# Kernel tuning notes

Hardware: AMD Instinct MI355X
Metric: run time of the kernel (lower is better)

Reference implementation:

```python
import jax, jax.numpy as jnp
import numpy as np
import math

B, N, D, H = 2, 2048, 512, 8
DH = D // H
HID = int(D * 16 / 3)  # 2730, SwiGLU hidden; chunks into 1365+1365
EPS = 1e-5


def _get_slopes(n):
    # n=8 is a power of two
    start = 2.0 ** (-2.0 ** (-(math.log2(n) - 3)))
    return np.array([start * (start ** i) for i in range(n)], dtype=np.float32)

_SLOPES = jnp.asarray(_get_slopes(H))  # [H]


def _ln(x, w, b):
    m = jnp.mean(x, axis=-1, keepdims=True)
    v = jnp.mean((x - m) ** 2, axis=-1, keepdims=True)
    return (x - m) * jax.lax.rsqrt(v + EPS) * w + b


def setup_inputs() -> dict:
    key = jax.random.key(0)
    ks = jax.random.split(key, 20)
    p = lambda k, s: jax.random.normal(k, s, jnp.float32) * 0.02
    return {
        "x": jax.random.normal(ks[0], (B, N, D), jnp.float32),
        "coords": jax.random.uniform(ks[1], (B, N, 2), jnp.float32) * 100.0,
        "q_w": p(ks[2], (D, D)), "q_b": jnp.zeros((D,), jnp.float32),
        "k_w": p(ks[3], (D, D)), "k_b": jnp.zeros((D,), jnp.float32),
        "v_w": p(ks[4], (D, D)), "v_b": jnp.zeros((D,), jnp.float32),
        "o_w": p(ks[5], (D, D)), "o_b": jnp.zeros((D,), jnp.float32),
        "gamma1": jnp.ones((D,), jnp.float32),
        "ln1_w": jnp.ones((D,), jnp.float32), "ln1_b": jnp.zeros((D,), jnp.float32),
        "fc1_w": p(ks[6], (HID, D)), "fc1_b": jnp.zeros((HID,), jnp.float32),
        "fc2_w": p(ks[7], (D, HID // 2)), "fc2_b": jnp.zeros((D,), jnp.float32),
        "gamma2": jnp.ones((D,), jnp.float32),
        "ln2_w": jnp.ones((D,), jnp.float32), "ln2_b": jnp.zeros((D,), jnp.float32),
    }


def reference(x, coords, q_w, q_b, k_w, k_b, v_w, v_b, o_w, o_b, gamma1,
              ln1_w, ln1_b, fc1_w, fc1_b, fc2_w, fc2_b, gamma2, ln2_w, ln2_b):
    # ---- residual1: distance-ALiBi attention (eval mode: x + gamma1*attn(norm(x)))
    xn = _ln(x, ln1_w, ln1_b)
    q = (xn @ q_w.T + q_b).reshape(B, N, H, DH).transpose(0, 2, 1, 3)  # [b,h,n,dh]
    k = (xn @ k_w.T + k_b).reshape(B, N, H, DH).transpose(0, 2, 1, 3)
    v = (xn @ v_w.T + v_b).reshape(B, N, H, DH).transpose(0, 2, 1, 3)
    # pairwise Euclidean distance of tile coords -> [b,n,n]
    diff = coords[:, :, None, :] - coords[:, None, :, :]
    dist = jnp.sqrt(jnp.sum(diff * diff, axis=-1))
    attn_bias = -_SLOPES[None, :, None, None] * dist[:, None, :, :]  # [b,h,n,n]
    scale = 1.0 / math.sqrt(DH)
    scores = jnp.einsum('bhqd,bhkd->bhqk', q, k) * scale + attn_bias
    attn = jax.nn.softmax(scores, axis=-1)
    ctx = jnp.einsum('bhqk,bhkd->bhqd', attn, v)
    ctx = ctx.transpose(0, 2, 1, 3).reshape(B, N, D)
    attn_out = ctx @ o_w.T + o_b
    x = x + gamma1 * attn_out
    # ---- residual2: SwiGLU-style MLP (eval mode: x + gamma2*mlp(norm(x)))
    xn2 = _ln(x, ln2_w, ln2_b)
    hpre = xn2 @ fc1_w.T + fc1_b  # [b,n,HID]
    h1, h2 = jnp.split(hpre, 2, axis=-1)
    mlp_out = (jax.nn.silu(h1) * h2) @ fc2_w.T + fc2_b
    return x + gamma2 * mlp_out
```

## Files before the change

### kernel.cpp

```cpp
#include <hip/hip_runtime.h>
#include <math.h>

#define Bdim  2
#define Nseq  2048
#define Dmod  512
#define Hn    8
#define DHd   64
#define HID   2730
#define HHALF 1365
#define HC    1408
#define NPACK 2816
#define ROWS  4096
#define NSPLIT 4
#define KT_PER (Nseq / 64 / NSPLIT)

typedef __bf16 bf16x8 __attribute__((ext_vector_type(8)));
typedef __bf16 bf16x4 __attribute__((ext_vector_type(4)));
typedef float  f32x4  __attribute__((ext_vector_type(4)));

__device__ __forceinline__ void glds16(const __bf16* g, __bf16* l) {
    __builtin_amdgcn_global_load_lds(
        (const __attribute__((address_space(1))) void*)g,
        (__attribute__((address_space(3))) void*)l, 16, 0, 0);
}

#define SEG0 (1536*512)
#define SEG1 (512*512)
#define SEG2 (NPACK*512)
#define SEG3 (512*HC)
__global__ __launch_bounds__(256) void convert_all(
    const float* __restrict__ q_w, const float* __restrict__ k_w,
    const float* __restrict__ v_w, const float* __restrict__ o_w,
    const float* __restrict__ fc1_w, const float* __restrict__ fc2_w,
    __bf16* __restrict__ wqkv, __bf16* __restrict__ wo,
    __bf16* __restrict__ wfc1p, __bf16* __restrict__ wfc2p)
{
    int idx = blockIdx.x * 256 + threadIdx.x;
    if (idx < SEG0) {
        int n = idx >> 9, k = idx & 511;
        float v = (n < 512) ? q_w[n * 512 + k]
                : (n < 1024) ? k_w[(n - 512) * 512 + k]
                : v_w[(n - 1024) * 512 + k];
        wqkv[idx] = (__bf16)v;
        return;
    }
    idx -= SEG0;
    if (idx < SEG1) { wo[idx] = (__bf16)o_w[idx]; return; }
    idx -= SEG1;
    if (idx < SEG2) {
        int n = idx >> 9, k = idx & 511;
        int j = n >> 5, u = n & 31;
        int base = j * 16 + (u & 15);
        float v = 0.0f;
        if (base < HHALF) {
            int hidx = base + ((u & 16) ? HHALF : 0);
            v = fc1_w[(size_t)hidx * 512 + k];
        }
        wfc1p[idx] = (__bf16)v;
        return;
    }
    idx -= SEG2;
    if (idx < SEG3) {
        int n = idx / HC, k = idx - n * HC;
        float v = (k < HHALF) ? fc2_w[(size_t)n * HHALF + k] : 0.0f;
        wfc2p[idx] = (__bf16)v;
    }
}

__global__ __launch_bounds__(256) void ln_kernel(
    const float* __restrict__ x, const float* __restrict__ w,
    const float* __restrict__ b, __bf16* __restrict__ out)
{
    const int row = blockIdx.x;
    const int tid = threadIdx.x;
    const float* xr = x + (size_t)row * Dmod;
    float2 v = *(const float2*)(xr + tid * 2);
    float s  = v.x + v.y;
    float sq = v.x * v.x + v.y * v.y;
#pragma unroll
    for (int m = 1; m < 64; m <<= 1) {
        s  += __shfl_xor(s, m, 64);
        sq += __shfl_xor(sq, m, 64);
    }
    __shared__ float ss[4], ssq[4];
    const int wv = tid >> 6;
    if ((tid & 63) == 0) { ss[wv] = s; ssq[wv] = sq; }
    __syncthreads();
    s  = ss[0] + ss[1] + ss[2] + ss[3];
    sq = ssq[0] + ssq[1] + ssq[2] + ssq[3];
    const float mean = s * (1.0f / Dmod);
    const float var  = sq * (1.0f / Dmod) - mean * mean;
    const float rstd = rsqrtf(var + 1e-5f);
    float2 wv2 = *(const float2*)(w + tid * 2);
    float2 bv2 = *(const float2*)(b + tid * 2);
    __bf16* orow = out + (size_t)row * Dmod + tid * 2;
    orow[0] = (__bf16)((v.x - mean) * rstd * wv2.x + bv2.x);
    orow[1] = (__bf16)((v.y - mean) * rstd * wv2.y + bv2.y);
}

__global__ __launch_bounds__(256) void gemm_res(
    const __bf16* __restrict__ A, int lda,
    const __bf16* __restrict__ Bw, int ldb,
    const float* __restrict__ bias, int K,
    float* __restrict__ out_f32, int ld_out,
    const float* __restrict__ res, const float* __restrict__ g)
{
    __shared__ __bf16 As[64 * 32];
    __shared__ __bf16 Bs[64 * 32];
    const int tid  = threadIdx.x;
    const int wave = tid >> 6, lane = tid & 63;
    const int t    = lane & 15, quad = lane >> 4;
    const int m0   = blockIdx.x * 64;
    const int n0   = blockIdx.y * 64;
    const int sr   = tid >> 2, sc = (tid & 3) * 8;

    f32x4 acc[4] = {};

    for (int k0 = 0; k0 < K; k0 += 32) {
        __syncthreads();
        glds16(A  + (size_t)(m0 + sr) * lda + k0 + sc, As + tid * 8);
        glds16(Bw + (size_t)(n0 + sr) * ldb + k0 + sc, Bs + tid * 8);
        __syncthreads();
        bf16x8 a = *(const bf16x8*)(As + (wave * 16 + t) * 32 + quad * 8);
#pragma unroll
        for (int ct = 0; ct < 4; ++ct) {
            bf16x8 b = *(const bf16x8*)(Bs + (ct * 16 + t) * 32 + quad * 8);
            acc[ct] = __builtin_amdgcn_mfma_f32_16x16x32_bf16(a, b, acc[ct], 0, 0, 0);
        }
    }

    const int row_base = m0 + wave * 16 + quad * 4;
#pragma unroll
    for (int ct = 0; ct < 4; ++ct) {
        const int col = n0 + ct * 16 + t;
        const float bb = bias[col];
#pragma unroll
        for (int r = 0; r < 4; ++r) {
            const int row = row_base + r;
            out_f32[(size_t)row * ld_out + col] =
                res[(size_t)row * ld_out + col] + g[col] * (acc[ct][r] + bb);
        }
    }
}

#define LDT 136
__global__ __launch_bounds__(256) void qkv_gemm128(
    const __bf16* __restrict__ A, const __bf16* __restrict__ W,
    const float* __restrict__ qb_, const float* __restrict__ kb_,
    const float* __restrict__ vb_,
    __bf16* __restrict__ qk, __bf16* __restrict__ vtg)
{
    __shared__ __bf16 smem[64 * LDT];
    __bf16* As = smem;
    __bf16* Bs = smem + 4096;
    const int tid  = threadIdx.x;
    const int wave = tid >> 6, lane = tid & 63;
    const int t    = lane & 15, quad = lane >> 4;
    const int m0   = blockIdx.x * 128, n0 = blockIdx.y * 128;
    const int mr   = (wave & 1) * 64,  nr = (wave >> 1) * 64;
    const int ra0 = tid >> 2,          ca0 = (tid & 3) * 8;
    const int ra1 = (tid + 256) >> 2,  ca1 = (tid & 3) * 8;

    f32x4 acc[4][4] = {};

    for (int k0 = 0; k0 < Dmod; k0 += 32) {
        __syncthreads();
        glds16(A + (size_t)(m0 + ra0) * Dmod + k0 + ca0, As + tid * 8);
        glds16(A + (size_t)(m0 + ra1) * Dmod + k0 + ca1, As + (tid + 256) * 8);
        glds16(W + (size_t)(n0 + ra0) * Dmod + k0 + ca0, Bs + tid * 8);
        glds16(W + (size_t)(n0 + ra1) * Dmod + k0 + ca1, Bs + (tid + 256) * 8);
        __syncthreads();
        bf16x8 af[4], bfr[4];
#pragma unroll
        for (int mi = 0; mi < 4; ++mi)
            af[mi] = *(const bf16x8*)(As + (mr + mi * 16 + t) * 32 + quad * 8);
#pragma unroll
        for (int ni = 0; ni < 4; ++ni)
            bfr[ni] = *(const bf16x8*)(Bs + (nr + ni * 16 + t) * 32 + quad * 8);
#pragma unroll
        for (int mi = 0; mi < 4; ++mi)
#pragma unroll
            for (int ni = 0; ni < 4; ++ni)
                acc[mi][ni] = __builtin_amdgcn_mfma_f32_16x16x32_bf16(af[mi], bfr[ni], acc[mi][ni], 0, 0, 0);
    }

    const int y = blockIdx.y;
    if (y < 8) {
#pragma unroll
        for (int mi = 0; mi < 4; ++mi) {
            const int row_base = m0 + mr + mi * 16 + quad * 4;
#pragma unroll
            for (int ni = 0; ni < 4; ++ni) {
                const int col = n0 + nr + ni * 16 + t;
                const float bb = (col < 512) ? qb_[col] : kb_[col - 512];
#pragma unroll
                for (int r = 0; r < 4; ++r)
                    qk[(size_t)(row_base + r) * 1024 + col] = (__bf16)(acc[mi][ni][r] + bb);
            }
        }
    } else {
        const int tok0 = m0 & 2047;
        const int bI   = m0 >> 11;
#pragma unroll
        for (int half = 0; half < 2; ++half) {
            __syncthreads();
            if ((wave >> 1) == half) {
#pragma unroll
                for (int ni = 0; ni < 4; ++ni) {
                    const int dh = ni * 16 + t;
                    const float bb = vb_[(y - 8) * 128 + half * 64 + dh];
#pragma unroll
                    for (int mi = 0; mi < 4; ++mi) {
                        const int n = mr + mi * 16 + quad * 4;
                        bf16x4 pk;
#pragma unroll
                        for (int r = 0; r < 4; ++r) pk[r] = (__bf16)(acc[mi][ni][r] + bb);
                        *(bf16x4*)(smem + dh * LDT + n) = pk;
                    }
                }
            }
            __syncthreads();
            const int hh = (y - 8) * 2 + half;
            const size_t rowbase = (size_t)(bI * 8 + hh) * 64;
#pragma unroll
            for (int j = 0; j < 4; ++j) {
                int chunk = tid + j * 256;
                int dr = chunk >> 4, cc = (chunk & 15) * 8;
                bf16x8 vv = *(const bf16x8*)(smem + dr * LDT + cc);
                *(bf16x8*)(vtg + (rowbase + dr) * Nseq + tok0 + cc) = vv;
            }
        }
    }
}

__global__ __launch_bounds__(256) void fc1_gemm128(
    const __bf16* __restrict__ A, const __bf16* __restrict__ W,
    const float* __restrict__ fc1_b_, __bf16* __restrict__ out)
{
    __shared__ __bf16 As[128 * 32];
    __shared__ __bf16 Bs[128 * 32];
    const int tid  = threadIdx.x;
    const int wave = tid >> 6, lane = tid & 63;
    const int t    = lane & 15, quad = lane >> 4;
    const int m0   = blockIdx.x * 128, n0 = blockIdx.y * 128;
    const int mr   = (wave & 1) * 64,  nr = (wave >> 1) * 64;
    const int ra0 = tid >> 2,          ca0 = (tid & 3) * 8;
    const int ra1 = (tid + 256) >> 2,  ca1 = (tid & 3) * 8;

    f32x4 acc[4][4] = {};

    for (int k0 = 0; k0 < Dmod; k0 += 32) {
        __syncthreads();
        glds16(A + (size_t)(m0 + ra0) * Dmod + k0 + ca0, As + tid * 8);
        glds16(A + (size_t)(m0 + ra1) * Dmod + k0 + ca1, As + (tid + 256) * 8);
        glds16(W + (size_t)(n0 + ra0) * Dmod + k0 + ca0, Bs + tid * 8);
        glds16(W + (size_t)(n0 + ra1) * Dmod + k0 + ca1, Bs + (tid + 256) * 8);
        __syncthreads();
        bf16x8 af[4], bfr[4];
#pragma unroll
        for (int mi = 0; mi < 4; ++mi)
            af[mi] = *(const bf16x8*)(As + (mr + mi * 16 + t) * 32 + quad * 8);
#pragma unroll
        for (int ni = 0; ni < 4; ++ni)
            bfr[ni] = *(const bf16x8*)(Bs + (nr + ni * 16 + t) * 32 + quad * 8);
#pragma unroll
        for (int mi = 0; mi < 4; ++mi)
#pragma unroll
            for (int ni = 0; ni < 4; ++ni)
                acc[mi][ni] = __builtin_amdgcn_mfma_f32_16x16x32_bf16(af[mi], bfr[ni], acc[mi][ni], 0, 0, 0);
    }

#pragma unroll
    for (int mi = 0; mi < 4; ++mi) {
        const int row_base = m0 + mr + mi * 16 + quad * 4;
#pragma unroll
        for (int gI = 0; gI < 2; ++gI) {
            const int base = n0 + nr + gI * 32;
            const int hb = (base >> 5) * 16 + t;
            const bool valid = hb < HHALF;
            const float b1 = valid ? fc1_b_[hb] : 0.0f;
            const float b2 = valid ? fc1_b_[HHALF + hb] : 0.0f;
#pragma unroll
            for (int r = 0; r < 4; ++r) {
                float a = acc[mi][2 * gI][r] + b1;
                float c = acc[mi][2 * gI + 1][r] + b2;
                float sw = a / (1.0f + __expf(-a)) * c;
                out[(size_t)(row_base + r) * HC + hb] = (__bf16)sw;
            }
        }
    }
}

__global__ __launch_bounds__(256) void attn_kernel(
    const __bf16* __restrict__ qk, const __bf16* __restrict__ vt,
    const float* __restrict__ coords,
    float* __restrict__ op, float* __restrict__ lp)
{
    constexpr int LD = 72;
    __shared__ __bf16 Ks[64][LD];
    __shared__ __bf16 Vt[64][LD];
    __shared__ __bf16 Ps[64][LD];
    __shared__ float2 kco[64];

    const int qt = blockIdx.x, h = blockIdx.y;
    const int s = blockIdx.z >> 1, b = blockIdx.z & 1;
    const int bh = b * Hn + h;
    const int tid = threadIdx.x;
    const int wave = tid >> 6, lane = tid & 63;
    const int t = lane & 15, quad = lane >> 4;
    const float c1 = 0.125f * 1.44269504f;
    const float d1 = exp2f(-(float)(h + 1)) * 1.44269504f;
    const int kt0 = s * KT_PER, kt1 = kt0 + KT_PER;

    const int qrow = qt * 64 + wave * 16 + t;
    const size_t qbase = (size_t)(b * Nseq + qrow) * 1024 + h * DHd;
    bf16x8 bq0 = *(const bf16x8*)(qk + qbase + quad * 8);
    bf16x8 bq1 = *(const bf16x8*)(qk + qbase + 32 + quad * 8);
    float2 qc = *(const float2*)(coords + (size_t)(b * Nseq + qrow) * 2);
    const float qx = qc.x, qy = qc.y;

    const int sr = tid >> 3, scc = (tid & 7) * 8;
    const __bf16* kbase = qk + (size_t)(b * Nseq) * 1024 + 512 + h * DHd;
    const __bf16* vbase = vt + (size_t)(bh * 64) * Nseq;

    bf16x8 kreg0, kreg1, vreg0, vreg1;
    float2 kcreg = {0.f, 0.f};
    {
        const int kn0 = kt0 * 64;
        kreg0 = *(const bf16x8*)(kbase + (size_t)(kn0 + sr) * 1024 + scc);
        kreg1 = *(const bf16x8*)(kbase + (size_t)(kn0 + sr + 32) * 1024 + scc);
        vreg0 = *(const bf16x8*)(vbase + (size_t)sr * Nseq + kn0 + scc);
        vreg1 = *(const bf16x8*)(vbase + (size_t)(sr + 32) * Nseq + kn0 + scc);
        if (tid < 64) kcreg = *(const float2*)(coords + (size_t)(b * Nseq + kn0 + tid) * 2);
    }

    f32x4 o[4] = {};
    float lrun = 0.0f;

    for (int kt = kt0; kt < kt1; ++kt) {
        __syncthreads();
        *(bf16x8*)(&Ks[sr][scc])      = kreg0;
        *(bf16x8*)(&Ks[sr + 32][scc]) = kreg1;
        *(bf16x8*)(&Vt[sr][scc])      = vreg0;
        *(bf16x8*)(&Vt[sr + 32][scc]) = vreg1;
        if (tid < 64) kco[tid] = kcreg;
        __syncthreads();
        if (kt + 1 < kt1) {
            const int kn = (kt + 1) * 64;
            kreg0 = *(const bf16x8*)(kbase + (size_t)(kn + sr) * 1024 + scc);
            kreg1 = *(const bf16x8*)(kbase + (size_t)(kn + sr + 32) * 1024 + scc);
            vreg0 = *(const bf16x8*)(vbase + (size_t)sr * Nseq + kn + scc);
            vreg1 = *(const bf16x8*)(vbase + (size_t)(sr + 32) * Nseq + kn + scc);
            if (tid < 64) kcreg = *(const float2*)(coords + (size_t)(b * Nseq + kn + tid) * 2);
        }

        f32x4 sA[4];
#pragma unroll
        for (int am = 0; am < 4; ++am) {
            bf16x8 a0 = *(const bf16x8*)(&Ks[am * 16 + t][quad * 8]);
            bf16x8 a1 = *(const bf16x8*)(&Ks[am * 16 + t][32 + quad * 8]);
            f32x4 z = {};
            z = __builtin_amdgcn_mfma_f32_16x16x32_bf16(a0, bq0, z, 0, 0, 0);
            sA[am] = __builtin_amdgcn_mfma_f32_16x16x32_bf16(a1, bq1, z, 0, 0, 0);
        }

        float p[4][4];
#pragma unroll
        for (int am = 0; am < 4; ++am)
#pragma unroll
            for (int r = 0; r < 4; ++r) {
                float2 kc = kco[am * 16 + quad * 4 + r];
                float dx = qx - kc.x, dy = qy - kc.y;
                float dist = __builtin_amdgcn_sqrtf(dx * dx + dy * dy);
                float e = __builtin_amdgcn_exp2f(sA[am][r] * c1 - d1 * dist);
                p[am][r] = e;
                lrun += e;
            }

#pragma unroll
        for (int am = 0; am < 4; ++am) {
            bf16x4 pk;
#pragma unroll
            for (int r = 0; r < 4; ++r) pk[r] = (__bf16)p[am][r];
            *(bf16x4*)(&Ps[wave * 16 + t][am * 16 + quad * 4]) = pk;
        }

        bf16x8 ap0 = *(const bf16x8*)(&Ps[wave * 16 + t][quad * 8]);
        bf16x8 ap1 = *(const bf16x8*)(&Ps[wave * 16 + t][32 + quad * 8]);
#pragma unroll
        for (int ct = 0; ct < 4; ++ct) {
            bf16x8 bv0 = *(const bf16x8*)(&Vt[ct * 16 + t][quad * 8]);
            bf16x8 bv1 = *(const bf16x8*)(&Vt[ct * 16 + t][32 + quad * 8]);
            o[ct] = __builtin_amdgcn_mfma_f32_16x16x32_bf16(ap0, bv0, o[ct], 0, 0, 0);
            o[ct] = __builtin_amdgcn_mfma_f32_16x16x32_bf16(ap1, bv1, o[ct], 0, 0, 0);
        }
    }

    lrun += __shfl_xor(lrun, 16, 64);
    lrun += __shfl_xor(lrun, 32, 64);
    if (quad == 0)
        lp[(((size_t)s * Bdim + b) * Hn + h) * Nseq + qt * 64 + wave * 16 + t] = lrun;

    const int orow_base = qt * 64 + wave * 16 + quad * 4;
#pragma unroll
    for (int ct = 0; ct < 4; ++ct)
#pragma unroll
        for (int r = 0; r < 4; ++r) {
            size_t row = (size_t)s * ROWS + b * Nseq + orow_base + r;
            op[row * Dmod + h * DHd + ct * 16 + t] = o[ct][r];
        }
}

__global__ __launch_bounds__(256) void merge_kernel(
    const float* __restrict__ op, const float* __restrict__ lp,
    __bf16* __restrict__ ctx)
{
    int idx = blockIdx.x * 256 + threadIdx.x;
    int row = idx >> 7, c4 = (idx & 127) * 4;
    int h = c4 >> 6;
    int b = row >> 11, n = row & 2047;
    float l = 0.0f;
#pragma unroll
    for (int s = 0; s < NSPLIT; ++s)
        l += lp[(((size_t)s * Bdim + b) * Hn + h) * Nseq + n];
    float rl = __builtin_amdgcn_rcpf(l);
    float4 oa = {0.f, 0.f, 0.f, 0.f};
#pragma unroll
    for (int s = 0; s < NSPLIT; ++s) {
        float4 ov = *(const float4*)(op + ((size_t)s * ROWS + row) * Dmod + c4);
        oa.x += ov.x; oa.y += ov.y; oa.z += ov.z; oa.w += ov.w;
    }
    bf16x4 r;
    r[0] = (__bf16)(oa.x * rl);
    r[1] = (__bf16)(oa.y * rl);
    r[2] = (__bf16)(oa.z * rl);
    r[3] = (__bf16)(oa.w * rl);
    *(bf16x4*)(ctx + (size_t)row * Dmod + c4) = r;
}

extern "C" void kernel_launch(void* const* d_in, const int* in_sizes, int n_in,
                              void* d_out, int out_size, void* d_ws, size_t ws_size,
                              hipStream_t stream)
{
    (void)in_sizes; (void)n_in; (void)out_size; (void)ws_size;
    const float* x      = (const float*)d_in[0];
    const float* coords = (const float*)d_in[1];
    const float* q_w    = (const float*)d_in[2];
    const float* q_b    = (const float*)d_in[3];
    const float* k_w    = (const float*)d_in[4];
    const float* k_b    = (const float*)d_in[5];
    const float* v_w    = (const float*)d_in[6];
    const float* v_b    = (const float*)d_in[7];
    const float* o_w    = (const float*)d_in[8];
    const float* o_b    = (const float*)d_in[9];
    const float* gamma1 = (const float*)d_in[10];
    const float* ln1_w  = (const float*)d_in[11];
    const float* ln1_b  = (const float*)d_in[12];
    const float* fc1_w  = (const float*)d_in[13];
    const float* fc1_b  = (const float*)d_in[14];
    const float* fc2_w  = (const float*)d_in[15];
    const float* fc2_b  = (const float*)d_in[16];
    const float* gamma2 = (const float*)d_in[17];
    const float* ln2_w  = (const float*)d_in[18];
    const float* ln2_b  = (const float*)d_in[19];

    size_t off = 0;
    auto alloc = [&](size_t bytes) {
        void* p = (char*)d_ws + off;
        off += (bytes + 255) & ~(size_t)255;
        return p;
    };
    __bf16* wqkv  = (__bf16*)alloc((size_t)1536 * 512 * 2);
    __bf16* wo    = (__bf16*)alloc((size_t)512 * 512 * 2);
    __bf16* wfc1p = (__bf16*)alloc((size_t)NPACK * 512 * 2);
    __bf16* wfc2p = (__bf16*)alloc((size_t)512 * HC * 2);
    __bf16* xn    = (__bf16*)alloc((size_t)ROWS * Dmod * 2);
    __bf16* xn2   = (__bf16*)alloc((size_t)ROWS * Dmod * 2);
    __bf16* qkb   = (__bf16*)alloc((size_t)ROWS * 1024 * 2);
    __bf16* vtg   = (__bf16*)alloc((size_t)Bdim * Hn * DHd * Nseq * 2);
    __bf16* ctxb  = (__bf16*)alloc((size_t)ROWS * Dmod * 2);
    float*  x1    = (float*)alloc((size_t)ROWS * Dmod * 4);
    __bf16* hcomb = (__bf16*)alloc((size_t)ROWS * HC * 2);
    float*  opb   = (float*)alloc((size_t)NSPLIT * ROWS * Dmod * 4);
    float*  lpb   = (float*)alloc((size_t)NSPLIT * Bdim * Hn * Nseq * 4);

    const int conv_total = SEG0 + SEG1 + SEG2 + SEG3;
    convert_all<<<(conv_total + 255) / 256, 256, 0, stream>>>(
        q_w, k_w, v_w, o_w, fc1_w, fc2_w, wqkv, wo, wfc1p, wfc2p);

    ln_kernel<<<ROWS, 256, 0, stream>>>(x, ln1_w, ln1_b, xn);

    qkv_gemm128<<<dim3(ROWS / 128, 12), 256, 0, stream>>>(xn, wqkv, q_b, k_b, v_b, qkb, vtg);

    attn_kernel<<<dim3(Nseq / 64, Hn, Bdim * NSPLIT), 256, 0, stream>>>(
        qkb, vtg, coords, opb, lpb);
    merge_kernel<<<(ROWS * 128 + 255) / 256, 256, 0, stream>>>(opb, lpb, ctxb);

    gemm_res<<<dim3(ROWS / 64, Dmod / 64), 256, 0, stream>>>(
        ctxb, Dmod, wo, Dmod, o_b, Dmod, x1, Dmod, x, gamma1);

    ln_kernel<<<ROWS, 256, 0, stream>>>(x1, ln2_w, ln2_b, xn2);

    fc1_gemm128<<<dim3(ROWS / 128, NPACK / 128), 256, 0, stream>>>(xn2, wfc1p, fc1_b, hcomb);

    gemm_res<<<dim3(ROWS / 64, Dmod / 64), 256, 0, stream>>>(
        hcomb, HC, wfc2p, HC, fc2_b, HC, (float*)d_out, Dmod, x1, gamma2);
}
```

Before: 236.7 us.

## Fuse weight conversion with LN1, split-K gemm_res, bf16 attention partials, fewer splits

```diff
diff --git a/kernel.cpp b/kernel.cpp
--- a/kernel.cpp
+++ b/kernel.cpp
@@ -11,7 +11,7 @@
 #define HC    1408
 #define NPACK 2816
 #define ROWS  4096
-#define NSPLIT 4
+#define NSPLIT 2
 #define KT_PER (Nseq / 64 / NSPLIT)
 
 typedef __bf16 bf16x8 __attribute__((ext_vector_type(8)));
@@ -24,55 +24,10 @@
         (__attribute__((address_space(3))) void*)l, 16, 0, 0);
 }
 
-#define SEG0 (1536*512)
-#define SEG1 (512*512)
-#define SEG2 (NPACK*512)
-#define SEG3 (512*HC)
-__global__ __launch_bounds__(256) void convert_all(
-    const float* __restrict__ q_w, const float* __restrict__ k_w,
-    const float* __restrict__ v_w, const float* __restrict__ o_w,
-    const float* __restrict__ fc1_w, const float* __restrict__ fc2_w,
-    __bf16* __restrict__ wqkv, __bf16* __restrict__ wo,
-    __bf16* __restrict__ wfc1p, __bf16* __restrict__ wfc2p)
-{
-    int idx = blockIdx.x * 256 + threadIdx.x;
-    if (idx < SEG0) {
-        int n = idx >> 9, k = idx & 511;
-        float v = (n < 512) ? q_w[n * 512 + k]
-                : (n < 1024) ? k_w[(n - 512) * 512 + k]
-                : v_w[(n - 1024) * 512 + k];
-        wqkv[idx] = (__bf16)v;
-        return;
-    }
-    idx -= SEG0;
-    if (idx < SEG1) { wo[idx] = (__bf16)o_w[idx]; return; }
-    idx -= SEG1;
-    if (idx < SEG2) {
-        int n = idx >> 9, k = idx & 511;
-        int j = n >> 5, u = n & 31;
-        int base = j * 16 + (u & 15);
-        float v = 0.0f;
-        if (base < HHALF) {
-            int hidx = base + ((u & 16) ? HHALF : 0);
-            v = fc1_w[(size_t)hidx * 512 + k];
-        }
-        wfc1p[idx] = (__bf16)v;
-        return;
-    }
-    idx -= SEG2;
-    if (idx < SEG3) {
-        int n = idx / HC, k = idx - n * HC;
-        float v = (k < HHALF) ? fc2_w[(size_t)n * HHALF + k] : 0.0f;
-        wfc2p[idx] = (__bf16)v;
-    }
-}
-
-__global__ __launch_bounds__(256) void ln_kernel(
-    const float* __restrict__ x, const float* __restrict__ w,
+__device__ __forceinline__ void ln_body(
+    int row, int tid, const float* __restrict__ x, const float* __restrict__ w,
     const float* __restrict__ b, __bf16* __restrict__ out)
 {
-    const int row = blockIdx.x;
-    const int tid = threadIdx.x;
     const float* xr = x + (size_t)row * Dmod;
     float2 v = *(const float2*)(xr + tid * 2);
     float s  = v.x + v.y;
@@ -98,47 +53,130 @@
     orow[1] = (__bf16)((v.y - mean) * rstd * wv2.y + bv2.y);
 }
 
-__global__ __launch_bounds__(256) void gemm_res(
+#define SEG0 (1536*512)
+#define SEG1 (512*512)
+#define SEG2 (NPACK*512)
+#define SEG3 (512*HC)
+#define CONV_BLOCKS ((SEG0 + SEG1 + SEG2 + SEG3) / 256)
+__global__ __launch_bounds__(256) void convert_ln(
+    const float* __restrict__ q_w, const float* __restrict__ k_w,
+    const float* __restrict__ v_w, const float* __restrict__ o_w,
+    const float* __restrict__ fc1_w, const float* __restrict__ fc2_w,
+    __bf16* __restrict__ wqkv, __bf16* __restrict__ wo,
+    __bf16* __restrict__ wfc1p, __bf16* __restrict__ wfc2p,
+    const float* __restrict__ x, const float* __restrict__ ln1w,
+    const float* __restrict__ ln1b, __bf16* __restrict__ xn)
+{
+    if (blockIdx.x >= CONV_BLOCKS) {
+        ln_body(blockIdx.x - CONV_BLOCKS, threadIdx.x, x, ln1w, ln1b, xn);
+        return;
+    }
+    int idx = blockIdx.x * 256 + threadIdx.x;
+    if (idx < SEG0) {
+        int n = idx >> 9, k = idx & 511;
+        float v = (n < 512) ? q_w[n * 512 + k]
+                : (n < 1024) ? k_w[(n - 512) * 512 + k]
+                : v_w[(n - 1024) * 512 + k];
+        wqkv[idx] = (__bf16)v;
+        return;
+    }
+    idx -= SEG0;
+    if (idx < SEG1) { wo[idx] = (__bf16)o_w[idx]; return; }
+    idx -= SEG1;
+    if (idx < SEG2) {
+        int n = idx >> 9, k = idx & 511;
+        int j = n >> 5, u = n & 31;
+        int base = j * 16 + (u & 15);
+        float v = 0.0f;
+        if (base < HHALF) {
+            int hidx = base + ((u & 16) ? HHALF : 0);
+            v = fc1_w[(size_t)hidx * 512 + k];
+        }
+        wfc1p[idx] = (__bf16)v;
+        return;
+    }
+    idx -= SEG2;
+    if (idx < SEG3) {
+        int n = idx / HC, k = idx - n * HC;
+        float v = (k < HHALF) ? fc2_w[(size_t)n * HHALF + k] : 0.0f;
+        wfc2p[idx] = (__bf16)v;
+    }
+}
+
+__global__ __launch_bounds__(256) void ln_kernel(
+    const float* __restrict__ x, const float* __restrict__ w,
+    const float* __restrict__ b, __bf16* __restrict__ out)
+{
+    ln_body(blockIdx.x, threadIdx.x, x, w, b, out);
+}
+
+__global__ __launch_bounds__(512) void gemm_res(
     const __bf16* __restrict__ A, int lda,
     const __bf16* __restrict__ Bw, int ldb,
     const float* __restrict__ bias, int K,
     float* __restrict__ out_f32, int ld_out,
     const float* __restrict__ res, const float* __restrict__ g)
 {
-    __shared__ __bf16 As[64 * 32];
-    __shared__ __bf16 Bs[64 * 32];
+    __shared__ __bf16 smem[2 * 64 * 64];
+    __bf16* As = smem;
+    __bf16* Bs = smem + 64 * 64;
     const int tid  = threadIdx.x;
     const int wave = tid >> 6, lane = tid & 63;
     const int t    = lane & 15, quad = lane >> 4;
+    const int kg   = wave >> 2, wv = wave & 3;
     const int m0   = blockIdx.x * 64;
     const int n0   = blockIdx.y * 64;
-    const int sr   = tid >> 2, sc = (tid & 3) * 8;
+
+    const int srow = tid >> 3;
+    const int gch  = ((tid & 7) ^ (srow & 7)) * 8;
+    const __bf16* aptr = A  + (size_t)(m0 + srow) * lda + gch;
+    const __bf16* bptr = Bw + (size_t)(n0 + srow) * ldb + gch;
+
+    const int arow = wv * 16 + t;
+    const int aoff = arow * 64 + (((kg * 4 + quad) ^ (arow & 7)) * 8);
+    int boffs[4];
+#pragma unroll
+    for (int ct = 0; ct < 4; ++ct) {
+        int brow = ct * 16 + t;
+        boffs[ct] = brow * 64 + (((kg * 4 + quad) ^ (brow & 7)) * 8);
+    }
 
     f32x4 acc[4] = {};
-
-    for (int k0 = 0; k0 < K; k0 += 32) {
-        __syncthreads();
-        glds16(A  + (size_t)(m0 + sr) * lda + k0 + sc, As + tid * 8);
-        glds16(Bw + (size_t)(n0 + sr) * ldb + k0 + sc, Bs + tid * 8);
-        __syncthreads();
-        bf16x8 a = *(const bf16x8*)(As + (wave * 16 + t) * 32 + quad * 8);
+    for (int k0 = 0; k0 < K; k0 += 64) {
+        __syncthreads();
+        glds16(aptr + k0, As + tid * 8);
+        glds16(bptr + k0, Bs + tid * 8);
+        __syncthreads();
+        bf16x8 a = *(const bf16x8*)(As + aoff);
 #pragma unroll
         for (int ct = 0; ct < 4; ++ct) {
-            bf16x8 b = *(const bf16x8*)(Bs + (ct * 16 + t) * 32 + quad * 8);
+            bf16x8 b = *(const bf16x8*)(Bs + boffs[ct]);
             acc[ct] = __builtin_amdgcn_mfma_f32_16x16x32_bf16(a, b, acc[ct], 0, 0, 0);
         }
     }
 
-    const int row_base = m0 + wave * 16 + quad * 4;
-#pragma unroll
-    for (int ct = 0; ct < 4; ++ct) {
-        const int col = n0 + ct * 16 + t;
-        const float bb = bias[col];
-#pragma unroll
-        for (int r = 0; r < 4; ++r) {
-            const int row = row_base + r;
-            out_f32[(size_t)row * ld_out + col] =
-                res[(size_t)row * ld_out + col] + g[col] * (acc[ct][r] + bb);
+    __syncthreads();
+    if (kg == 1) {
+        float* dst = (float*)smem + ((size_t)wv * 64 + lane) * 16;
+#pragma unroll
+        for (int ct = 0; ct < 4; ++ct) *(f32x4*)(dst + ct * 4) = acc[ct];
+    }
+    __syncthreads();
+    if (kg == 0) {
+        const float* src = (const float*)smem + ((size_t)wv * 64 + lane) * 16;
+        const int row_base = m0 + wv * 16 + quad * 4;
+#pragma unroll
+        for (int ct = 0; ct < 4; ++ct) {
+            f32x4 other = *(const f32x4*)(src + ct * 4);
+            const int col = n0 + ct * 16 + t;
+            const float bb = bias[col];
+#pragma unroll
+            for (int r = 0; r < 4; ++r) {
+                const int row = row_base + r;
+                out_f32[(size_t)row * ld_out + col] =
+                    res[(size_t)row * ld_out + col] +
+                    g[col] * (acc[ct][r] + other[r] + bb);
+            }
         }
     }
 }
@@ -294,7 +332,7 @@
 __global__ __launch_bounds__(256) void attn_kernel(
     const __bf16* __restrict__ qk, const __bf16* __restrict__ vt,
     const float* __restrict__ coords,
-    float* __restrict__ op, float* __restrict__ lp)
+    __bf16* __restrict__ op, float* __restrict__ lp)
 {
     constexpr int LD = 72;
     __shared__ __bf16 Ks[64][LD];
@@ -407,12 +445,12 @@
 #pragma unroll
         for (int r = 0; r < 4; ++r) {
             size_t row = (size_t)s * ROWS + b * Nseq + orow_base + r;
-            op[row * Dmod + h * DHd + ct * 16 + t] = o[ct][r];
+            op[row * Dmod + h * DHd + ct * 16 + t] = (__bf16)o[ct][r];
         }
 }
 
 __global__ __launch_bounds__(256) void merge_kernel(
-    const float* __restrict__ op, const float* __restrict__ lp,
+    const __bf16* __restrict__ op, const float* __restrict__ lp,
     __bf16* __restrict__ ctx)
 {
     int idx = blockIdx.x * 256 + threadIdx.x;
@@ -424,17 +462,16 @@
     for (int s = 0; s < NSPLIT; ++s)
         l += lp[(((size_t)s * Bdim + b) * Hn + h) * Nseq + n];
     float rl = __builtin_amdgcn_rcpf(l);
-    float4 oa = {0.f, 0.f, 0.f, 0.f};
+    float oa[4] = {0.f, 0.f, 0.f, 0.f};
 #pragma unroll
     for (int s = 0; s < NSPLIT; ++s) {
-        float4 ov = *(const float4*)(op + ((size_t)s * ROWS + row) * Dmod + c4);
-        oa.x += ov.x; oa.y += ov.y; oa.z += ov.z; oa.w += ov.w;
+        bf16x4 ov = *(const bf16x4*)(op + ((size_t)s * ROWS + row) * Dmod + c4);
+#pragma unroll
+        for (int j = 0; j < 4; ++j) oa[j] += (float)ov[j];
     }
     bf16x4 r;
-    r[0] = (__bf16)(oa.x * rl);
-    r[1] = (__bf16)(oa.y * rl);
-    r[2] = (__bf16)(oa.z * rl);
-    r[3] = (__bf16)(oa.w * rl);
+#pragma unroll
+    for (int j = 0; j < 4; ++j) r[j] = (__bf16)(oa[j] * rl);
     *(bf16x4*)(ctx + (size_t)row * Dmod + c4) = r;
 }
 
@@ -481,14 +518,12 @@
     __bf16* ctxb  = (__bf16*)alloc((size_t)ROWS * Dmod * 2);
     float*  x1    = (float*)alloc((size_t)ROWS * Dmod * 4);
     __bf16* hcomb = (__bf16*)alloc((size_t)ROWS * HC * 2);
-    float*  opb   = (float*)alloc((size_t)NSPLIT * ROWS * Dmod * 4);
+    __bf16* opb   = (__bf16*)alloc((size_t)NSPLIT * ROWS * Dmod * 2);
     float*  lpb   = (float*)alloc((size_t)NSPLIT * Bdim * Hn * Nseq * 4);
 
-    const int conv_total = SEG0 + SEG1 + SEG2 + SEG3;
-    convert_all<<<(conv_total + 255) / 256, 256, 0, stream>>>(
-        q_w, k_w, v_w, o_w, fc1_w, fc2_w, wqkv, wo, wfc1p, wfc2p);
-
-    ln_kernel<<<ROWS, 256, 0, stream>>>(x, ln1_w, ln1_b, xn);
+    convert_ln<<<CONV_BLOCKS + ROWS, 256, 0, stream>>>(
+        q_w, k_w, v_w, o_w, fc1_w, fc2_w, wqkv, wo, wfc1p, wfc2p,
+        x, ln1_w, ln1_b, xn);
 
     qkv_gemm128<<<dim3(ROWS / 128, 12), 256, 0, stream>>>(xn, wqkv, q_b, k_b, v_b, qkb, vtg);
 
@@ -496,13 +531,13 @@
         qkb, vtg, coords, opb, lpb);
     merge_kernel<<<(ROWS * 128 + 255) / 256, 256, 0, stream>>>(opb, lpb, ctxb);
 
-    gemm_res<<<dim3(ROWS / 64, Dmod / 64), 256, 0, stream>>>(
+    gemm_res<<<dim3(ROWS / 64, Dmod / 64), 512, 0, stream>>>(
         ctxb, Dmod, wo, Dmod, o_b, Dmod, x1, Dmod, x, gamma1);
 
     ln_kernel<<<ROWS, 256, 0, stream>>>(x1, ln2_w, ln2_b, xn2);
 
     fc1_gemm128<<<dim3(ROWS / 128, NPACK / 128), 256, 0, stream>>>(xn2, wfc1p, fc1_b, hcomb);
 
-    gemm_res<<<dim3(ROWS / 64, Dmod / 64), 256, 0, stream>>>(
+    gemm_res<<<dim3(ROWS / 64, Dmod / 64), 512, 0, stream>>>(
         hcomb, HC, wfc2p, HC, fc2_b, HC, (float*)d_out, Dmod, x1, gamma2);
 }
```

Result: faster. 218.4 us (-7.7%).
